# Kernel optimization log

Measured on AMD Instinct MI355X. Metric: run time of the kernel, lower is better.

## Reference

```python
import jax, jax.numpy as jnp
import numpy as np

N_NODES, N_EDGES, N_GRAPHS = 200000, 6400000, 64


def setup_inputs() -> dict:
    key = jax.random.key(0)
    ks = jax.random.split(key, 8)
    rij = jax.random.normal(ks[0], (N_EDGES, 3), jnp.float32)
    fij = jax.random.normal(ks[1], (N_EDGES, 3), jnp.float32)
    pos_grad = jax.random.normal(ks[2], (N_NODES, 3), jnp.float32)
    cell_grad = jax.random.normal(ks[3], (N_GRAPHS, 3, 3), jnp.float32)
    les_cell = jax.random.normal(ks[4], (N_GRAPHS, 3, 3), jnp.float32)
    cell_volume = jax.random.uniform(ks[5], (N_GRAPHS,), jnp.float32) + 0.5  # positive volumes
    edge_idx = jax.random.randint(ks[6], (2, N_EDGES), 0, N_NODES, dtype=jnp.int32)
    batch = jnp.sort(jax.random.randint(ks[7], (N_NODES,), 0, N_GRAPHS, dtype=jnp.int32))
    return {
        "rij": rij, "fij": fij, "pos_grad": pos_grad, "cell_grad": cell_grad,
        "les_cell": les_cell, "cell_volume": cell_volume, "edge_idx": edge_idx,
        "batch": batch, "n_nodes": N_NODES, "n_graphs": N_GRAPHS,
    }


def reference(rij, fij, pos_grad, cell_grad, les_cell, cell_volume, edge_idx, batch, n_nodes, n_graphs):
    seg = jax.ops.segment_sum
    # Path 1: edge-gradient forces (pf - nf), minus Path 2 positional grad.
    pf = seg(fij, edge_idx[0], num_segments=n_nodes)          # [N,3]
    nf = seg(fij, edge_idx[1], num_segments=n_nodes)          # [N,3]
    force = pf - nf - pos_grad                                 # [N,3]
    # Edge virial in Voigt-like order [xx,yy,zz,xy,yz,zx].
    diag = rij * fij                                           # [E,3]
    virial = jnp.concatenate([
        diag,
        (rij[:, 0] * fij[:, 1])[:, None],
        (rij[:, 1] * fij[:, 2])[:, None],
        (rij[:, 2] * fij[:, 0])[:, None],
    ], axis=-1)                                                # [E,6]
    s_node = seg(virial, edge_idx[1], num_segments=n_nodes)    # [N,6] atomic virial
    sout = seg(s_node, batch, num_segments=n_graphs)           # [B,6]
    stress = -sout / cell_volume[:, None]                      # [B,6]
    # Path 3: Ewald cell stress sigma_lr = -(1/V) cell^T @ dE/dcell.
    lr = -(jnp.swapaxes(les_cell, -2, -1) @ cell_grad) / cell_volume[:, None, None]
    lr_voigt = jnp.stack([lr[:, 0, 0], lr[:, 1, 1], lr[:, 2, 2],
                          lr[:, 0, 1], lr[:, 1, 2], lr[:, 0, 2]], axis=-1)
    return force, stress + lr_voigt
```

## Files before the change

### kernel.cpp

```cpp
#include <hip/hip_runtime.h>
#include <hip/hip_fp16.h>

static constexpr int TPB       = 256;
static constexpr int MAXB      = 64;
static constexpr int BIN_SHIFT = 12;
static constexpr int BINSZ     = 1 << BIN_SHIFT;
static constexpr int SUB_SHIFT = 11;
static constexpr int SUBSZ     = 1 << SUB_SHIFT;
static constexpr int NSUB      = BINSZ / SUBSZ;
static constexpr int CAP       = 64;
static constexpr int CAPB      = 176;
static constexpr int NBLKS     = 2048;
static constexpr int SSL       = 16;
static constexpr int BPS       = NBLKS / SSL;
static constexpr int MAXG      = 64;
static constexpr int SLOTS     = MAXG * 6;
static constexpr int NWAVES    = TPB / 64;

static constexpr float VSCALE  = 4096.0f;
static constexpr float VINV    = 1.0f / 4096.0f;
static constexpr float FSCALE  = 1048576.0f;
static constexpr float FINV    = 1.0f / 1048576.0f;
static constexpr float OSCALE  = 65536.0f;
static constexpr float OINV    = 1.0f / 65536.0f;

__global__ __launch_bounds__(TPB) void zero_ovf_kernel(int4* __restrict__ p4, long n4) {
    long i = (long)blockIdx.x * TPB + threadIdx.x;
    const long gs = (long)gridDim.x * TPB;
    for (; i < n4; i += gs) p4[i] = make_int4(0, 0, 0, 0);
}

__device__ inline uint2 pack_rec(int node, float fx, float fy, float fz) {
    unsigned lid = (unsigned)node & (BINSZ - 1);
    unsigned w0 = (unsigned)__half_as_ushort(__float2half(fx)) |
                  ((unsigned)__half_as_ushort(__float2half(fy)) << 16);
    unsigned w1 = (unsigned)__half_as_ushort(__float2half(fz)) | (lid << 16);
    return make_uint2(w0, w1);
}

__device__ inline void ovf_add(int* __restrict__ ovf, int node,
                               float fx, float fy, float fz) {
    atomicAdd(&ovf[3 * node + 0], __float2int_rn(fx * OSCALE));
    atomicAdd(&ovf[3 * node + 1], __float2int_rn(fy * OSCALE));
    atomicAdd(&ovf[3 * node + 2], __float2int_rn(fz * OSCALE));
}

__global__ __launch_bounds__(TPB) void scatter_kernel(
    const float* __restrict__ rij, const float* __restrict__ fij,
    const int* __restrict__ idx0, const int* __restrict__ idx1,
    const int* __restrict__ batch,
    uint2* __restrict__ rec, unsigned* __restrict__ cnt_out,
    int* __restrict__ ovf, float* __restrict__ apart,
    int E, int nbins) {
    extern __shared__ char smem[];
    uint2* buf = (uint2*)smem;
    unsigned* cnt = (unsigned*)(buf + (size_t)nbins * CAP);
    unsigned* loc = cnt + nbins;
    int* s_acc = (int*)(loc + nbins);

    for (int t = threadIdx.x; t < nbins; t += TPB) { cnt[t] = 0u; loc[t] = 0u; }
    for (int t = threadIdx.x; t < SLOTS; t += TPB) s_acc[t] = 0;
    __syncthreads();

    const int NG = E >> 2;
    const int GC = (NG + NBLKS - 1) / NBLKS;
    const int g0 = blockIdx.x * GC;
    int g1 = g0 + GC; if (g1 > NG) g1 = NG;
    const int span = g1 - g0;
    const int niter = span > 0 ? (span + TPB - 1) / TPB : 0;

    const float4* fij4 = (const float4*)fij;
    const float4* rij4 = (const float4*)rij;
    const int4* i04 = (const int4*)idx0;
    const int4* i14 = (const int4*)idx1;

    const int wid = threadIdx.x >> 6, lane = threadIdx.x & 63;

    for (int it = 0; it < niter; ++it) {
        int k = g0 + it * TPB + threadIdx.x;
        if (k < g1) {
            float4 fa = fij4[3 * k], fb = fij4[3 * k + 1], fc = fij4[3 * k + 2];
            float4 ra = rij4[3 * k], rb = rij4[3 * k + 1], rc = rij4[3 * k + 2];
            int4 i0 = i04[k], i1 = i14[k];
            float fx[4] = {fa.x, fa.w, fb.z, fc.y};
            float fy[4] = {fa.y, fb.x, fb.w, fc.z};
            float fz[4] = {fa.z, fb.y, fc.x, fc.w};
            float rx[4] = {ra.x, ra.w, rb.z, rc.y};
            float ry[4] = {ra.y, rb.x, rb.w, rc.z};
            float rz[4] = {ra.z, rb.y, rc.x, rc.w};
            int s[4] = {i0.x, i0.y, i0.z, i0.w};
            int r[4] = {i1.x, i1.y, i1.z, i1.w};

            int bb[8]; uint2 wv[8]; unsigned slot[8];
#pragma unroll
            for (int e = 0; e < 4; ++e) {
                bb[2 * e] = s[e] >> BIN_SHIFT;
                wv[2 * e] = pack_rec(s[e], fx[e], fy[e], fz[e]);
                bb[2 * e + 1] = r[e] >> BIN_SHIFT;
                wv[2 * e + 1] = pack_rec(r[e], -fx[e], -fy[e], -fz[e]);
            }
#pragma unroll
            for (int j = 0; j < 8; ++j)
                slot[j] = atomicAdd(&cnt[bb[j]], 1u);
#pragma unroll
            for (int j = 0; j < 8; ++j) {
                if (slot[j] < (unsigned)CAP) {
                    buf[bb[j] * CAP + slot[j]] = wv[j];
                } else {
                    int node = (bb[j] << BIN_SHIFT) | (int)(wv[j].y >> 16);
                    float ox = __half2float(__ushort_as_half((unsigned short)(wv[j].x & 0xffffu)));
                    float oy = __half2float(__ushort_as_half((unsigned short)(wv[j].x >> 16)));
                    float oz = __half2float(__ushort_as_half((unsigned short)(wv[j].y & 0xffffu)));
                    ovf_add(ovf, node, ox, oy, oz);
                }
            }
#pragma unroll
            for (int e = 0; e < 4; ++e) {
                int g = batch[r[e]];
                int* a = &s_acc[6 * g];
                atomicAdd(&a[0], __float2int_rn(rx[e] * fx[e] * VSCALE));
                atomicAdd(&a[1], __float2int_rn(ry[e] * fy[e] * VSCALE));
                atomicAdd(&a[2], __float2int_rn(rz[e] * fz[e] * VSCALE));
                atomicAdd(&a[3], __float2int_rn(rx[e] * fy[e] * VSCALE));
                atomicAdd(&a[4], __float2int_rn(ry[e] * fz[e] * VSCALE));
                atomicAdd(&a[5], __float2int_rn(rz[e] * fx[e] * VSCALE));
            }
        }
        __syncthreads();
        for (int b = wid; b < nbins; b += NWAVES) {
            unsigned c = cnt[b];
            unsigned m = c < (unsigned)CAP ? c : (unsigned)CAP;
            unsigned off0 = loc[b];
            if ((unsigned)lane < m) {
                unsigned sl_ = off0 + (unsigned)lane;
                uint2 w = buf[b * CAP + lane];
                if (sl_ < (unsigned)CAPB) {
                    rec[((size_t)b * NBLKS + blockIdx.x) * CAPB + sl_] = w;
                } else {
                    int node = (b << BIN_SHIFT) | (int)(w.y >> 16);
                    float ox = __half2float(__ushort_as_half((unsigned short)(w.x & 0xffffu)));
                    float oy = __half2float(__ushort_as_half((unsigned short)(w.x >> 16)));
                    float oz = __half2float(__ushort_as_half((unsigned short)(w.y & 0xffffu)));
                    ovf_add(ovf, node, ox, oy, oz);
                }
            }
            if (lane == 0) {
                unsigned no = off0 + m;
                loc[b] = no < (unsigned)CAPB ? no : (unsigned)CAPB;
                cnt[b] = 0u;
            }
        }
        __syncthreads();
    }

    if (blockIdx.x == 0) {
        for (int e = (NG << 2) + threadIdx.x; e < E; e += TPB) {
            float gx = fij[3 * e], gy = fij[3 * e + 1], gz = fij[3 * e + 2];
            int si = idx0[e], ri = idx1[e];
            ovf_add(ovf, si, gx, gy, gz);
            ovf_add(ovf, ri, -gx, -gy, -gz);
            float ex = rij[3 * e], ey = rij[3 * e + 1], ez = rij[3 * e + 2];
            int g = batch[ri];
            int* a = &s_acc[6 * g];
            atomicAdd(&a[0], __float2int_rn(ex * gx * VSCALE));
            atomicAdd(&a[1], __float2int_rn(ey * gy * VSCALE));
            atomicAdd(&a[2], __float2int_rn(ez * gz * VSCALE));
            atomicAdd(&a[3], __float2int_rn(ex * gy * VSCALE));
            atomicAdd(&a[4], __float2int_rn(ey * gz * VSCALE));
            atomicAdd(&a[5], __float2int_rn(ez * gx * VSCALE));
        }
    }

    __syncthreads();
    for (int t = threadIdx.x; t < nbins; t += TPB)
        cnt_out[(size_t)t * NBLKS + blockIdx.x] = loc[t];
    for (int t = threadIdx.x; t < SLOTS; t += TPB)
        apart[(size_t)t * NBLKS + blockIdx.x] = (float)s_acc[t] * VINV;
}

__global__ __launch_bounds__(TPB) void bin_accum_kernel(
    const uint2* __restrict__ rec, const unsigned* __restrict__ cnt_out,
    float* __restrict__ bpart) {
    __shared__ int lf[SUBSZ * 3];
    __shared__ unsigned scnt[BPS];
    const int sl = blockIdx.x % SSL;
    const int r2 = blockIdx.x / SSL;
    const int st = r2 & (NSUB - 1);
    const int bin = r2 >> 1;
    const int b0 = sl * BPS;

    int4* lf4 = (int4*)lf;
    for (int t = threadIdx.x; t < SUBSZ * 3 / 4; t += TPB)
        lf4[t] = make_int4(0, 0, 0, 0);
    for (int t = threadIdx.x; t < BPS; t += TPB)
        scnt[t] = cnt_out[(size_t)bin * NBLKS + b0 + t];
    __syncthreads();

    const int wid = threadIdx.x >> 6, lane = threadIdx.x & 63;

    for (int blk = wid; blk < BPS; blk += NWAVES) {
        unsigned c = scnt[blk];
        size_t base = ((size_t)bin * NBLKS + (b0 + blk)) * CAPB;
        for (unsigned r = (unsigned)lane; r < c; r += 64) {
            uint2 w = rec[base + r];
            unsigned lid = w.y >> 16;
            if ((int)(lid >> SUB_SHIFT) == st) {
                unsigned l2 = lid & (SUBSZ - 1);
                float fx = __half2float(__ushort_as_half((unsigned short)(w.x & 0xffffu)));
                float fy = __half2float(__ushort_as_half((unsigned short)(w.x >> 16)));
                float fz = __half2float(__ushort_as_half((unsigned short)(w.y & 0xffffu)));
                atomicAdd(&lf[l2 * 3 + 0], __float2int_rn(fx * FSCALE));
                atomicAdd(&lf[l2 * 3 + 1], __float2int_rn(fy * FSCALE));
                atomicAdd(&lf[l2 * 3 + 2], __float2int_rn(fz * FSCALE));
            }
        }
    }
    __syncthreads();
    float4* dst = (float4*)(bpart + (size_t)blockIdx.x * (SUBSZ * 3));
    for (int t = threadIdx.x; t < SUBSZ * 3 / 4; t += TPB) {
        int4 v = lf4[t];
        dst[t] = make_float4((float)v.x * FINV, (float)v.y * FINV,
                             (float)v.z * FINV, (float)v.w * FINV);
    }
}

__global__ __launch_bounds__(TPB) void force_kernel(
    const float* __restrict__ bpart, const int* __restrict__ ovf,
    const float* __restrict__ pos_grad,
    float* __restrict__ force, long n3) {
    long j = (long)blockIdx.x * TPB + threadIdx.x;
    const long gs = (long)gridDim.x * TPB;
    for (; j < n3; j += gs) {
        unsigned i = (unsigned)(j / 3);
        unsigned c = (unsigned)(j - 3L * i);
        unsigned bin = i >> BIN_SHIFT;
        unsigned st = (i >> SUB_SHIFT) & (NSUB - 1);
        unsigned l2 = i & (SUBSZ - 1);
        float acc = -pos_grad[j] + (float)ovf[j] * OINV;
        size_t tb = ((size_t)(bin * NSUB + st) * SSL) * (SUBSZ * 3) + l2 * 3 + c;
#pragma unroll
        for (int sl = 0; sl < SSL; ++sl)
            acc += bpart[tb + (size_t)sl * (SUBSZ * 3)];
        force[j] = acc;
    }
}

__global__ __launch_bounds__(TPB) void stress_kernel(
    const float* __restrict__ apart,
    const float* __restrict__ cell_grad, const float* __restrict__ les_cell,
    const float* __restrict__ vol, float* __restrict__ stress, int slots) {
    int t = blockIdx.x;
    if (t >= slots) return;
    __shared__ float red[TPB];
    float s = 0.f;
    const float* row = apart + (size_t)t * NBLKS;
    for (int j = threadIdx.x; j < NBLKS; j += TPB) s += row[j];
    red[threadIdx.x] = s;
    __syncthreads();
    for (int w = TPB / 2; w > 0; w >>= 1) {
        if (threadIdx.x < w) red[threadIdx.x] += red[threadIdx.x + w];
        __syncthreads();
    }
    if (threadIdx.x == 0) {
        int g = t / 6, c = t - 6 * g;
        const int va[6] = {0, 1, 2, 0, 1, 0};
        const int vb[6] = {0, 1, 2, 1, 2, 2};
        int a = va[c], bb = vb[c];
        const float* L = les_cell + 9 * g;
        const float* Gm = cell_grad + 9 * g;
        float lr = L[a] * Gm[bb] + L[3 + a] * Gm[3 + bb] + L[6 + a] * Gm[6 + bb];
        stress[t] = (-red[0] - lr) / vol[g];
    }
}

__global__ void init_force_kernel(const float4* __restrict__ pg4,
                                  float4* __restrict__ f4, int n4,
                                  const float* __restrict__ pg,
                                  float* __restrict__ f, int n) {
    int i = blockIdx.x * blockDim.x + threadIdx.x;
    int s = gridDim.x * blockDim.x;
    for (int k = i; k < n4; k += s) {
        float4 v = pg4[k];
        f4[k] = make_float4(-v.x, -v.y, -v.z, -v.w);
    }
    for (int k = n4 * 4 + i; k < n; k += s) f[k] = -pg[k];
}

__global__ __launch_bounds__(256) void edge_dev_kernel(
    const float* __restrict__ rij, const float* __restrict__ fij,
    const int* __restrict__ idx0, const int* __restrict__ idx1,
    const int* __restrict__ batch,
    float* __restrict__ force, float* __restrict__ partials, int E) {
    __shared__ float s_acc[SLOTS];
    for (int t = threadIdx.x; t < SLOTS; t += blockDim.x) s_acc[t] = 0.0f;
    __syncthreads();
    const int stride = gridDim.x * blockDim.x;
    const int tid0 = blockIdx.x * blockDim.x + threadIdx.x;
    for (int e = tid0; e < E; e += stride) {
        float ex = rij[3 * e], ey = rij[3 * e + 1], ez = rij[3 * e + 2];
        float gx = fij[3 * e], gy = fij[3 * e + 1], gz = fij[3 * e + 2];
        int si = idx0[e], ri = idx1[e];
        atomicAdd(&force[3 * si + 0], gx);
        atomicAdd(&force[3 * si + 1], gy);
        atomicAdd(&force[3 * si + 2], gz);
        atomicAdd(&force[3 * ri + 0], -gx);
        atomicAdd(&force[3 * ri + 1], -gy);
        atomicAdd(&force[3 * ri + 2], -gz);
        int g = batch[ri];
        float* a = &s_acc[6 * g];
        atomicAdd(&a[0], ex * gx);
        atomicAdd(&a[1], ey * gy);
        atomicAdd(&a[2], ez * gz);
        atomicAdd(&a[3], ex * gy);
        atomicAdd(&a[4], ey * gz);
        atomicAdd(&a[5], ez * gx);
    }
    __syncthreads();
    for (int t = threadIdx.x; t < SLOTS; t += blockDim.x)
        partials[(size_t)blockIdx.x * SLOTS + t] = s_acc[t];
}

__global__ void reduce_finalize_kernel(const float* __restrict__ partials, int nblocks,
                                       const float* __restrict__ cell_grad,
                                       const float* __restrict__ les_cell,
                                       const float* __restrict__ vol,
                                       float* __restrict__ stress_out, int slots) {
    int t = blockIdx.x * blockDim.x + threadIdx.x;
    if (t >= slots) return;
    float s = 0.0f;
    for (int b = 0; b < nblocks; ++b) s += partials[(size_t)b * SLOTS + t];
    int g = t / 6, c = t - 6 * g;
    const int va[6] = {0, 1, 2, 0, 1, 0};
    const int vb[6] = {0, 1, 2, 1, 2, 2};
    int a = va[c], bb = vb[c];
    const float* L = les_cell + 9 * g;
    const float* G = cell_grad + 9 * g;
    float lr = L[a] * G[bb] + L[3 + a] * G[3 + bb] + L[6 + a] * G[6 + bb];
    stress_out[t] = (-s - lr) / vol[g];
}

static inline size_t alignup(size_t x) { return (x + 255) & ~(size_t)255; }

extern "C" void kernel_launch(void* const* d_in, const int* in_sizes, int n_in,
                              void* d_out, int out_size, void* d_ws, size_t ws_size,
                              hipStream_t stream) {
    const float* rij = (const float*)d_in[0];
    const float* fij = (const float*)d_in[1];
    const float* pos_grad = (const float*)d_in[2];
    const float* cell_grad = (const float*)d_in[3];
    const float* les_cell = (const float*)d_in[4];
    const float* vol = (const float*)d_in[5];
    const int* edge_idx = (const int*)d_in[6];
    const int* batch = (const int*)d_in[7];

    const int E = in_sizes[0] / 3;
    const int N = in_sizes[2] / 3;
    const int ngr = in_sizes[5];
    const int slots = 6 * ngr;

    float* force = (float*)d_out;
    float* stress = (float*)d_out + (size_t)N * 3;

    const int nbins = (N + BINSZ - 1) >> BIN_SHIFT;
    const long N3 = (long)N * 3;

    const size_t rec_elems = (size_t)nbins * NBLKS * CAPB;

    size_t off = 0;
    const size_t o_rec = off;    off += alignup(rec_elems * 8);
    const size_t o_cnt = off;    off += alignup((size_t)nbins * NBLKS * 4);
    const size_t o_ovf = off;    off += alignup(((size_t)N3 + 4) * 4);
    const size_t o_apart = off;  off += alignup((size_t)SLOTS * NBLKS * 4);
    const size_t o_bpart = off;  off += alignup((size_t)nbins * NSUB * SSL * (SUBSZ * 3) * 4);
    const bool fit = (off <= ws_size) && (nbins <= MAXB) && (ngr <= MAXG) && (E >= 4);

    if (fit) {
        char* ws = (char*)d_ws;
        uint2* rec = (uint2*)(ws + o_rec);
        unsigned* cnt_out = (unsigned*)(ws + o_cnt);
        int* ovf = (int*)(ws + o_ovf);
        float* apart = (float*)(ws + o_apart);
        float* bpart = (float*)(ws + o_bpart);

        long n4 = (N3 + 3) / 4;
        int zb = (int)((n4 + TPB - 1) / TPB); if (zb > 2048) zb = 2048; if (zb < 1) zb = 1;
        zero_ovf_kernel<<<zb, TPB, 0, stream>>>((int4*)ovf, n4);

        const size_t smem = (size_t)nbins * CAP * 8 + (size_t)nbins * 8 + SLOTS * 4;
        scatter_kernel<<<NBLKS, TPB, smem, stream>>>(
            rij, fij, edge_idx, edge_idx + E, batch, rec, cnt_out, ovf, apart,
            E, nbins);

        bin_accum_kernel<<<nbins * NSUB * SSL, TPB, 0, stream>>>(rec, cnt_out, bpart);

        int fblocks = (int)((N3 + TPB - 1) / TPB);
        if (fblocks > 4096) fblocks = 4096;
        force_kernel<<<fblocks, TPB, 0, stream>>>(bpart, ovf, pos_grad, force, N3);

        stress_kernel<<<slots, TPB, 0, stream>>>(apart, cell_grad, les_cell, vol,
                                                 stress, slots);
    } else {
        float* partials = (float*)d_ws;
        int eblocks = 512;
        size_t need = (size_t)eblocks * SLOTS * sizeof(float);
        if (need > ws_size) {
            int fit2 = (int)(ws_size / (SLOTS * sizeof(float)));
            eblocks = fit2 > 0 ? fit2 : 1;
        }
        int n = (int)N3, n4 = n / 4;
        int blocks = (n4 + 255) / 256;
        if (blocks > 1024) blocks = 1024;
        if (blocks < 1) blocks = 1;
        init_force_kernel<<<blocks, 256, 0, stream>>>(
            (const float4*)pos_grad, (float4*)force, n4, pos_grad, force, n);
        edge_dev_kernel<<<eblocks, 256, 0, stream>>>(rij, fij, edge_idx, edge_idx + E,
                                                     batch, force, partials, E);
        reduce_finalize_kernel<<<6, 64, 0, stream>>>(partials, eblocks, cell_grad,
                                                     les_cell, vol, stress, slots);
    }
}
```

Before: 216.6 us.

## Write scatter records directly to global bins, drop LDS staging buffer

```diff
diff --git a/kernel.cpp b/kernel.cpp
--- a/kernel.cpp
+++ b/kernel.cpp
@@ -8,7 +8,6 @@
 static constexpr int SUB_SHIFT = 11;
 static constexpr int SUBSZ     = 1 << SUB_SHIFT;
 static constexpr int NSUB      = BINSZ / SUBSZ;
-static constexpr int CAP       = 64;
 static constexpr int CAPB      = 176;
 static constexpr int NBLKS     = 2048;
 static constexpr int SSL       = 16;
@@ -52,105 +51,77 @@
     uint2* __restrict__ rec, unsigned* __restrict__ cnt_out,
     int* __restrict__ ovf, float* __restrict__ apart,
     int E, int nbins) {
-    extern __shared__ char smem[];
-    uint2* buf = (uint2*)smem;
-    unsigned* cnt = (unsigned*)(buf + (size_t)nbins * CAP);
-    unsigned* loc = cnt + nbins;
-    int* s_acc = (int*)(loc + nbins);
-
-    for (int t = threadIdx.x; t < nbins; t += TPB) { cnt[t] = 0u; loc[t] = 0u; }
-    for (int t = threadIdx.x; t < SLOTS; t += TPB) s_acc[t] = 0;
+    __shared__ unsigned loc[MAXB];
+    __shared__ int s_acc[NWAVES][SLOTS];
+
+    for (int t = threadIdx.x; t < nbins; t += TPB) loc[t] = 0u;
+    for (int t = threadIdx.x; t < NWAVES * SLOTS; t += TPB)
+        ((int*)s_acc)[t] = 0;
     __syncthreads();
 
     const int NG = E >> 2;
     const int GC = (NG + NBLKS - 1) / NBLKS;
     const int g0 = blockIdx.x * GC;
     int g1 = g0 + GC; if (g1 > NG) g1 = NG;
-    const int span = g1 - g0;
-    const int niter = span > 0 ? (span + TPB - 1) / TPB : 0;
 
     const float4* fij4 = (const float4*)fij;
     const float4* rij4 = (const float4*)rij;
     const int4* i04 = (const int4*)idx0;
     const int4* i14 = (const int4*)idx1;
 
-    const int wid = threadIdx.x >> 6, lane = threadIdx.x & 63;
-
-    for (int it = 0; it < niter; ++it) {
-        int k = g0 + it * TPB + threadIdx.x;
-        if (k < g1) {
-            float4 fa = fij4[3 * k], fb = fij4[3 * k + 1], fc = fij4[3 * k + 2];
-            float4 ra = rij4[3 * k], rb = rij4[3 * k + 1], rc = rij4[3 * k + 2];
-            int4 i0 = i04[k], i1 = i14[k];
-            float fx[4] = {fa.x, fa.w, fb.z, fc.y};
-            float fy[4] = {fa.y, fb.x, fb.w, fc.z};
-            float fz[4] = {fa.z, fb.y, fc.x, fc.w};
-            float rx[4] = {ra.x, ra.w, rb.z, rc.y};
-            float ry[4] = {ra.y, rb.x, rb.w, rc.z};
-            float rz[4] = {ra.z, rb.y, rc.x, rc.w};
-            int s[4] = {i0.x, i0.y, i0.z, i0.w};
-            int r[4] = {i1.x, i1.y, i1.z, i1.w};
-
-            int bb[8]; uint2 wv[8]; unsigned slot[8];
-#pragma unroll
-            for (int e = 0; e < 4; ++e) {
-                bb[2 * e] = s[e] >> BIN_SHIFT;
-                wv[2 * e] = pack_rec(s[e], fx[e], fy[e], fz[e]);
-                bb[2 * e + 1] = r[e] >> BIN_SHIFT;
-                wv[2 * e + 1] = pack_rec(r[e], -fx[e], -fy[e], -fz[e]);
+    const int wid = threadIdx.x >> 6;
+    int* my_acc = s_acc[wid];
+
+    for (int k = g0 + threadIdx.x; k < g1; k += TPB) {
+        int4 i0 = i04[k], i1 = i14[k];
+        int s[4] = {i0.x, i0.y, i0.z, i0.w};
+        int r[4] = {i1.x, i1.y, i1.z, i1.w};
+        int gg[4];
+#pragma unroll
+        for (int e = 0; e < 4; ++e) gg[e] = batch[r[e]];
+
+        float4 fa = fij4[3 * k], fb = fij4[3 * k + 1], fc = fij4[3 * k + 2];
+        float4 ra = rij4[3 * k], rb = rij4[3 * k + 1], rc = rij4[3 * k + 2];
+        float fx[4] = {fa.x, fa.w, fb.z, fc.y};
+        float fy[4] = {fa.y, fb.x, fb.w, fc.z};
+        float fz[4] = {fa.z, fb.y, fc.x, fc.w};
+        float rx[4] = {ra.x, ra.w, rb.z, rc.y};
+        float ry[4] = {ra.y, rb.x, rb.w, rc.z};
+        float rz[4] = {ra.z, rb.y, rc.x, rc.w};
+
+        int bb[8]; uint2 wv[8]; unsigned slot[8];
+#pragma unroll
+        for (int e = 0; e < 4; ++e) {
+            bb[2 * e] = s[e] >> BIN_SHIFT;
+            wv[2 * e] = pack_rec(s[e], fx[e], fy[e], fz[e]);
+            bb[2 * e + 1] = r[e] >> BIN_SHIFT;
+            wv[2 * e + 1] = pack_rec(r[e], -fx[e], -fy[e], -fz[e]);
+        }
+#pragma unroll
+        for (int j = 0; j < 8; ++j)
+            slot[j] = atomicAdd(&loc[bb[j]], 1u);
+#pragma unroll
+        for (int j = 0; j < 8; ++j) {
+            if (slot[j] < (unsigned)CAPB) {
+                rec[((size_t)bb[j] * NBLKS + blockIdx.x) * CAPB + slot[j]] = wv[j];
+            } else {
+                int node = (bb[j] << BIN_SHIFT) | (int)(wv[j].y >> 16);
+                float ox = __half2float(__ushort_as_half((unsigned short)(wv[j].x & 0xffffu)));
+                float oy = __half2float(__ushort_as_half((unsigned short)(wv[j].x >> 16)));
+                float oz = __half2float(__ushort_as_half((unsigned short)(wv[j].y & 0xffffu)));
+                ovf_add(ovf, node, ox, oy, oz);
             }
-#pragma unroll
-            for (int j = 0; j < 8; ++j)
-                slot[j] = atomicAdd(&cnt[bb[j]], 1u);
-#pragma unroll
-            for (int j = 0; j < 8; ++j) {
-                if (slot[j] < (unsigned)CAP) {
-                    buf[bb[j] * CAP + slot[j]] = wv[j];
-                } else {
-                    int node = (bb[j] << BIN_SHIFT) | (int)(wv[j].y >> 16);
-                    float ox = __half2float(__ushort_as_half((unsigned short)(wv[j].x & 0xffffu)));
-                    float oy = __half2float(__ushort_as_half((unsigned short)(wv[j].x >> 16)));
-                    float oz = __half2float(__ushort_as_half((unsigned short)(wv[j].y & 0xffffu)));
-                    ovf_add(ovf, node, ox, oy, oz);
-                }
-            }
-#pragma unroll
-            for (int e = 0; e < 4; ++e) {
-                int g = batch[r[e]];
-                int* a = &s_acc[6 * g];
-                atomicAdd(&a[0], __float2int_rn(rx[e] * fx[e] * VSCALE));
-                atomicAdd(&a[1], __float2int_rn(ry[e] * fy[e] * VSCALE));
-                atomicAdd(&a[2], __float2int_rn(rz[e] * fz[e] * VSCALE));
-                atomicAdd(&a[3], __float2int_rn(rx[e] * fy[e] * VSCALE));
-                atomicAdd(&a[4], __float2int_rn(ry[e] * fz[e] * VSCALE));
-                atomicAdd(&a[5], __float2int_rn(rz[e] * fx[e] * VSCALE));
-            }
-        }
-        __syncthreads();
-        for (int b = wid; b < nbins; b += NWAVES) {
-            unsigned c = cnt[b];
-            unsigned m = c < (unsigned)CAP ? c : (unsigned)CAP;
-            unsigned off0 = loc[b];
-            if ((unsigned)lane < m) {
-                unsigned sl_ = off0 + (unsigned)lane;
-                uint2 w = buf[b * CAP + lane];
-                if (sl_ < (unsigned)CAPB) {
-                    rec[((size_t)b * NBLKS + blockIdx.x) * CAPB + sl_] = w;
-                } else {
-                    int node = (b << BIN_SHIFT) | (int)(w.y >> 16);
-                    float ox = __half2float(__ushort_as_half((unsigned short)(w.x & 0xffffu)));
-                    float oy = __half2float(__ushort_as_half((unsigned short)(w.x >> 16)));
-                    float oz = __half2float(__ushort_as_half((unsigned short)(w.y & 0xffffu)));
-                    ovf_add(ovf, node, ox, oy, oz);
-                }
-            }
-            if (lane == 0) {
-                unsigned no = off0 + m;
-                loc[b] = no < (unsigned)CAPB ? no : (unsigned)CAPB;
-                cnt[b] = 0u;
-            }
-        }
-        __syncthreads();
+        }
+#pragma unroll
+        for (int e = 0; e < 4; ++e) {
+            int* a = &my_acc[6 * gg[e]];
+            atomicAdd(&a[0], __float2int_rn(rx[e] * fx[e] * VSCALE));
+            atomicAdd(&a[1], __float2int_rn(ry[e] * fy[e] * VSCALE));
+            atomicAdd(&a[2], __float2int_rn(rz[e] * fz[e] * VSCALE));
+            atomicAdd(&a[3], __float2int_rn(rx[e] * fy[e] * VSCALE));
+            atomicAdd(&a[4], __float2int_rn(ry[e] * fz[e] * VSCALE));
+            atomicAdd(&a[5], __float2int_rn(rz[e] * fx[e] * VSCALE));
+        }
     }
 
     if (blockIdx.x == 0) {
@@ -161,7 +132,7 @@
             ovf_add(ovf, ri, -gx, -gy, -gz);
             float ex = rij[3 * e], ey = rij[3 * e + 1], ez = rij[3 * e + 2];
             int g = batch[ri];
-            int* a = &s_acc[6 * g];
+            int* a = &my_acc[6 * g];
             atomicAdd(&a[0], __float2int_rn(ex * gx * VSCALE));
             atomicAdd(&a[1], __float2int_rn(ey * gy * VSCALE));
             atomicAdd(&a[2], __float2int_rn(ez * gz * VSCALE));
@@ -172,10 +143,14 @@
     }
 
     __syncthreads();
-    for (int t = threadIdx.x; t < nbins; t += TPB)
-        cnt_out[(size_t)t * NBLKS + blockIdx.x] = loc[t];
-    for (int t = threadIdx.x; t < SLOTS; t += TPB)
-        apart[(size_t)t * NBLKS + blockIdx.x] = (float)s_acc[t] * VINV;
+    for (int t = threadIdx.x; t < nbins; t += TPB) {
+        unsigned c = loc[t];
+        cnt_out[(size_t)t * NBLKS + blockIdx.x] = c < (unsigned)CAPB ? c : (unsigned)CAPB;
+    }
+    for (int t = threadIdx.x; t < SLOTS; t += TPB) {
+        int v = s_acc[0][t] + s_acc[1][t] + s_acc[2][t] + s_acc[3][t];
+        apart[(size_t)t * NBLKS + blockIdx.x] = (float)v * VINV;
+    }
 }
 
 __global__ __launch_bounds__(TPB) void bin_accum_kernel(
@@ -386,8 +361,7 @@
         int zb = (int)((n4 + TPB - 1) / TPB); if (zb > 2048) zb = 2048; if (zb < 1) zb = 1;
         zero_ovf_kernel<<<zb, TPB, 0, stream>>>((int4*)ovf, n4);
 
-        const size_t smem = (size_t)nbins * CAP * 8 + (size_t)nbins * 8 + SLOTS * 4;
-        scatter_kernel<<<NBLKS, TPB, smem, stream>>>(
+        scatter_kernel<<<NBLKS, TPB, 0, stream>>>(
             rij, fij, edge_idx, edge_idx + E, batch, rec, cnt_out, ovf, apart,
             E, nbins);
 
```

After: 257.6 us. 18.9% more time.
